# Performance work log

Measured on AMD Instinct MI355X. Metric: run time of the kernel, lower is better.

## Reference

```python
import jax, jax.numpy as jnp
import numpy as np

NQ = 10000   # num_q
N = 512      # n (seq len)
D = 512      # d (model dim)
H = 8        # attention heads
LW = 64      # local window
B = 16       # batch


def _mha(q, k, v, wi, bi, wo, bo, nh, mask=None):
    # torch nn.MultiheadAttention math (eval mode, dropout off), batch-first inputs
    Bq, S, d = q.shape
    hd = d // nh
    wq, wk, wv = jnp.split(wi, 3, axis=0)
    bq, bk, bv = jnp.split(bi, 3)

    def proj(x, w, b):
        y = x @ w.T + b
        return y.reshape(x.shape[0], x.shape[1], nh, hd).transpose(0, 2, 1, 3)  # [B,h,S,hd]

    Q = proj(q, wq, bq)
    K = proj(k, wk, bk)
    V = proj(v, wv, bv)
    s = jnp.einsum('bhqe,bhke->bhqk', Q, K) / jnp.sqrt(jnp.asarray(hd, q.dtype))
    if mask is not None:
        s = jnp.where(mask[None, None], -jnp.inf, s)
    w = jax.nn.softmax(s, axis=-1)
    o = jnp.einsum('bhqk,bhke->bhqe', w, V).transpose(0, 2, 1, 3).reshape(Bq, S, d)
    return o @ wo.T + bo, w.mean(axis=1)  # avg over heads like torch default


def _ln(x, g, b):
    m = x.mean(-1, keepdims=True)
    v = ((x - m) ** 2).mean(-1, keepdims=True)
    return (x - m) / jnp.sqrt(v + 1e-5) * g + b


def setup_inputs() -> dict:
    key = jax.random.key(0)
    ks = iter(jax.random.split(key, 40))
    f = lambda *sh: jax.random.normal(next(ks), sh, jnp.float32) * 0.02
    inp = {
        'q': jax.random.randint(next(ks), (B, N), 0, NQ, jnp.int32),
        'r': jax.random.randint(next(ks), (B, N), 0, 2, jnp.int32),
        'qry': jax.random.randint(next(ks), (B, N), 0, NQ, jnp.int32),
        'M_emb': f(2 * NQ, D),
        'E_emb': f(NQ, D),
        'P': f(N, D),
    }
    for nm in ['base', 'local', 'glob', 'cross']:
        inp[nm + '_in_w'] = f(3 * D, D)
        inp[nm + '_in_b'] = jnp.zeros((3 * D,), jnp.float32)
        inp[nm + '_out_w'] = f(D, D)
        inp[nm + '_out_b'] = jnp.zeros((D,), jnp.float32)
    inp['ln1_g'] = jnp.ones((D,), jnp.float32)
    inp['ln1_b'] = jnp.zeros((D,), jnp.float32)
    inp['w1'] = f(D, D)
    inp['b1'] = jnp.zeros((D,), jnp.float32)
    inp['w2'] = f(D, D)
    inp['b2'] = jnp.zeros((D,), jnp.float32)
    inp['ln2_g'] = jnp.ones((D,), jnp.float32)
    inp['ln2_b'] = jnp.zeros((D,), jnp.float32)
    inp['pred_w'] = f(1, D)
    inp['pred_b'] = jnp.zeros((1,), jnp.float32)
    return inp


def reference(q, r, qry, M_emb, E_emb, P,
              base_in_w, base_in_b, base_out_w, base_out_b,
              local_in_w, local_in_b, local_out_w, local_out_b,
              glob_in_w, glob_in_b, glob_out_w, glob_out_b,
              cross_in_w, cross_in_b, cross_out_w, cross_out_b,
              ln1_g, ln1_b, w1, b1, w2, b2, ln2_g, ln2_b, pred_w, pred_b):
    x = q + NQ * r
    M = M_emb[x] + P[None]          # [B,N,D], positional added as in torch code
    E = E_emb[qry]                  # [B,N,D]
    cm = jnp.triu(jnp.ones((N, N), bool), 1)

    S_base, attn_w = _mha(E, M, M, base_in_w, base_in_b, base_out_w, base_out_b, H, cm)
    S_base = _ln(S_base + M + E, ln1_g, ln1_b)

    lm = jnp.triu(jnp.ones((LW, LW), bool), 1)
    s_loc_in = S_base[:, -LW:, :]
    S_loc, _ = _mha(s_loc_in, s_loc_in, s_loc_in, local_in_w, local_in_b, local_out_w, local_out_b, H, lm)
    S_local = jnp.concatenate([jnp.zeros((S_base.shape[0], N - LW, D), S_base.dtype), S_loc], axis=1)

    S_global, _ = _mha(S_base, S_base, S_base, glob_in_w, glob_in_b, glob_out_w, glob_out_b, H, cm)
    S_cross, _ = _mha(S_base, S_local, S_local, cross_in_w, cross_in_b, cross_out_w, cross_out_b, H, None)

    S = S_base + S_local + S_global + S_cross
    F = jax.nn.relu(S @ w1.T + b1) @ w2.T + b2
    F = _ln(F + S, ln2_g, ln2_b)
    p = jax.nn.sigmoid(F @ pred_w.T + pred_b)[..., 0]   # [B,N]
    return p, attn_w
```

## Files before the change

kernel.cpp:

```cpp
#include <hip/hip_runtime.h>
#include <hip/hip_bf16.h>

#define D_MODEL 512
#define NHEAD 8
#define NSEQ 512
#define BATCH 16
#define LWIN 64
#define S2C 0.18033688f
#define L2E 1.44269504f

typedef short s16x8 __attribute__((ext_vector_type(8)));
typedef float f32x4 __attribute__((ext_vector_type(4)));

__device__ inline unsigned short f2bf(float f) {
    unsigned int u = __float_as_uint(f);
    u = (u + 0x7fffu + ((u >> 16) & 1u)) >> 16;
    return (unsigned short)u;
}
__device__ inline int sw4(int r) { return (r + (r >> 2)) & 3; }

#define GLD16(g, l) __builtin_amdgcn_global_load_lds( \
    (const __attribute__((address_space(1))) void*)(g), \
    (__attribute__((address_space(3))) void*)(l), 16, 0, 0)

struct WP { const float* p[10]; };
__global__ __launch_bounds__(256) void wconv_kernel(WP wp, unsigned short* __restrict__ Wb)
{
    const long e = ((long)blockIdx.x * 256 + threadIdx.x) * 4;
    const float* src; long loc;
    if (e < 3145728) { int rg = (int)(e / 786432); src = wp.p[rg]; loc = e - (long)rg * 786432; }
    else { long j = e - 3145728; int rg = (int)(j >> 18); src = wp.p[4 + rg]; loc = j - ((long)rg << 18); }
    float4 v = *(const float4*)(src + loc);
    ushort4 o; o.x = f2bf(v.x); o.y = f2bf(v.y); o.z = f2bf(v.z); o.w = f2bf(v.w);
    *(ushort4*)(Wb + e) = o;
}

__global__ __launch_bounds__(128) void embed_kernel(
    const int* __restrict__ q, const int* __restrict__ r, const int* __restrict__ qry,
    const float* __restrict__ M_emb, const float* __restrict__ E_emb,
    const float* __restrict__ P, float* __restrict__ Mf, float* __restrict__ Ef,
    unsigned short* __restrict__ Mb, unsigned short* __restrict__ Eb)
{
    const int t = blockIdx.x;
    const int n = t & (NSEQ - 1);
    const int x = q[t] + 10000 * r[t];
    const int e = qry[t];
    const int i = threadIdx.x;
    float4 a = ((const float4*)(M_emb + (long)x * D_MODEL))[i];
    float4 p4 = ((const float4*)(P + (long)n * D_MODEL))[i];
    float4 ev = ((const float4*)(E_emb + (long)e * D_MODEL))[i];
    float4 mv = make_float4(a.x + p4.x, a.y + p4.y, a.z + p4.z, a.w + p4.w);
    ((float4*)(Mf + (long)t * D_MODEL))[i] = mv;
    ((float4*)(Ef + (long)t * D_MODEL))[i] = ev;
    ushort4 mb; mb.x = f2bf(mv.x); mb.y = f2bf(mv.y); mb.z = f2bf(mv.z); mb.w = f2bf(mv.w);
    ushort4 eb; eb.x = f2bf(ev.x); eb.y = f2bf(ev.y); eb.z = f2bf(ev.z); eb.w = f2bf(ev.w);
    *(ushort4*)(Mb + (long)t * D_MODEL + i * 4) = mb;
    *(ushort4*)(Eb + (long)t * D_MODEL + i * 4) = eb;
}

__global__ __launch_bounds__(256) void zfill_kernel(unsigned short* __restrict__ p)
{
    const long i = ((long)blockIdx.x * 256 + threadIdx.x) * 8;
    *(uint4*)(p + i) = make_uint4(0u, 0u, 0u, 0u);
}

__global__ __launch_bounds__(256) void gemm_bf16(
    const unsigned short* __restrict__ A, const unsigned short* __restrict__ A2, int nsplit,
    const unsigned short* __restrict__ W, const float* __restrict__ bias,
    unsigned short* __restrict__ Cb, int ldcb, int crem,
    float* __restrict__ Cf, int ldcf,
    const float* __restrict__ r1, const float* __restrict__ r2, const float* __restrict__ tl,
    int relu, int arem)
{
    __shared__ __align__(16) unsigned short Sh[6144];
    unsigned short* As = Sh;
    unsigned short* Ws = Sh + 4096;
    float* Shf = (float*)Sh;

    const int tid = threadIdx.x, lane = tid & 63, wid = tid >> 6;
    const int m0 = blockIdx.y * 128, n0 = blockIdx.x * 64;
    const int lm = lane & 15;
    const int lq = lane >> 4;
    const unsigned short* Asel = (n0 >= nsplit) ? A2 : A;

    const int rlane = lane >> 2, clane = lane & 3;
    const int lr0 = wid * 16 + rlane;
    const int lr1 = 64 + lr0;
    int rgA0 = m0 + lr0, rgA1 = m0 + lr1;
    if (arem) {
        rgA0 = ((rgA0 >> 6) << 9) + (NSEQ - LWIN) + (rgA0 & 63);
        rgA1 = ((rgA1 >> 6) << 9) + (NSEQ - LWIN) + (rgA1 & 63);
    }
    const unsigned short* pA0 = Asel + (long)rgA0 * 512 + ((clane ^ sw4(lr0)) << 3);
    const unsigned short* pA1 = Asel + (long)rgA1 * 512 + ((clane ^ sw4(lr1)) << 3);
    const unsigned short* pW0 = W + (long)(n0 + lr0) * 512 + ((clane ^ sw4(lr0)) << 3);
    unsigned short* lA0 = As + (wid * 16) * 32;
    unsigned short* lA1 = As + (64 + wid * 16) * 32;
    unsigned short* lW0 = Ws + (wid * 16) * 32;

    f32x4 acc[2][4];
    #pragma unroll
    for (int i = 0; i < 2; ++i)
        #pragma unroll
        for (int j = 0; j < 4; ++j) acc[i][j] = (f32x4){0.f, 0.f, 0.f, 0.f};

    for (int k0 = 0; k0 < 512; k0 += 32) {
        __syncthreads();
        GLD16(pA0 + k0, lA0);
        GLD16(pA1 + k0, lA1);
        GLD16(pW0 + k0, lW0);
        __syncthreads();

        s16x8 af[2], wf[4];
        #pragma unroll
        for (int i = 0; i < 2; ++i) {
            const int ra = wid * 32 + i * 16 + lm;
            af[i] = *(const s16x8*)&As[ra * 32 + ((lq ^ sw4(ra)) << 3)];
        }
        #pragma unroll
        for (int j = 0; j < 4; ++j) {
            const int rw = j * 16 + lm;
            wf[j] = *(const s16x8*)&Ws[rw * 32 + ((lq ^ sw4(rw)) << 3)];
        }
        #pragma unroll
        for (int i = 0; i < 2; ++i)
            #pragma unroll
            for (int j = 0; j < 4; ++j)
                acc[i][j] = __builtin_amdgcn_mfma_f32_16x16x32_bf16(af[i], wf[j], acc[i][j], 0, 0, 0);
    }

    const int fr = lane & 15;
    const int q4 = (lane >> 4) * 4;
    for (int qtr = 0; qtr < 4; ++qtr) {
        __syncthreads();
        if (wid == qtr) {
            #pragma unroll
            for (int j = 0; j < 4; ++j) {
                const int lcol = j * 16 + fr;
                const float bv = bias[n0 + lcol];
                #pragma unroll
                for (int i = 0; i < 2; ++i) {
                    #pragma unroll
                    for (int rg = 0; rg < 4; ++rg) {
                        float v = acc[i][j][rg] + bv;
                        if (relu) v = fmaxf(v, 0.f);
                        Shf[(i * 16 + q4 + rg) * 68 + lcol] = v;
                    }
                }
            }
        }
        __syncthreads();
        #pragma unroll
        for (int it = 0; it < 2; ++it) {
            const int flat = it * 256 + tid;
            const int rowq = flat >> 4, k4 = flat & 15;
            const int grow = m0 + qtr * 32 + rowq;
            const int gcol = n0 + k4 * 4;
            float4 f = *(const float4*)&Shf[rowq * 68 + k4 * 4];
            if (r1) {
                float4 a = *(const float4*)(r1 + (long)grow * 512 + gcol);
                float4 b = *(const float4*)(r2 + (long)grow * 512 + gcol);
                f.x += a.x + b.x; f.y += a.y + b.y; f.z += a.z + b.z; f.w += a.w + b.w;
                const int n = grow & 511;
                if (n >= NSEQ - LWIN) {
                    float4 c = *(const float4*)(tl + ((long)(grow >> 9) * 64 + (n - (NSEQ - LWIN))) * 512 + gcol);
                    f.x += c.x; f.y += c.y; f.z += c.z; f.w += c.w;
                }
            }
            if (Cf) *(float4*)(Cf + (long)grow * ldcf + gcol) = f;
            if (Cb) {
                const int crow = crem ? (((grow >> 6) << 9) + (NSEQ - LWIN) + (grow & 63)) : grow;
                ushort4 u; u.x = f2bf(f.x); u.y = f2bf(f.y); u.z = f2bf(f.z); u.w = f2bf(f.w);
                *(ushort4*)(Cb + (long)crow * ldcb + gcol) = u;
            }
        }
    }
}

__global__ __launch_bounds__(256) void flash_mfma(
    const unsigned short* __restrict__ Q, const unsigned short* __restrict__ K,
    const unsigned short* __restrict__ V, unsigned short* __restrict__ O,
    float* __restrict__ stats, int Nq, int Nkv, int ldq, int ldkv, int causal)
{
    __shared__ __align__(16) unsigned short Ks[64 * 72];
    __shared__ __align__(16) unsigned short Pl[64 * 72];
    __shared__ __align__(16) unsigned int   Vt[64 * 36];

    const int tid = threadIdx.x, lane = tid & 63, w = tid >> 6;
    const int lm = lane & 15, lq = lane >> 4;
    const int h = blockIdx.y, b = blockIdx.z;
    const int nqt = Nq >> 6;
    const int qa = blockIdx.x, qb = nqt - 1 - qa;
    const bool single = (qa == qb);

    s16x8 aqA0, aqA1, aqB0, aqB1;
    {
        const unsigned short* qp = Q + ((long)b * Nq + qb * 64 + w * 16 + lm) * ldq + h * 64 + lq * 8;
        aqB0 = *(const s16x8*)qp; aqB1 = *(const s16x8*)(qp + 32);
    }
    if (!single) {
        const unsigned short* qp = Q + ((long)b * Nq + qa * 64 + w * 16 + lm) * ldq + h * 64 + lq * 8;
        aqA0 = *(const s16x8*)qp; aqA1 = *(const s16x8*)(qp + 32);
    }

    float mA = -INFINITY, lA = 0.f, mB = -INFINITY, lB = 0.f;
    f32x4 oA[4], oB[4];
    #pragma unroll
    for (int t = 0; t < 4; ++t) { oA[t] = (f32x4){0.f,0.f,0.f,0.f}; oB[t] = (f32x4){0.f,0.f,0.f,0.f}; }

    const int nkt = causal ? (qb + 1) : (Nkv >> 6);
    const int skey = tid >> 3, sd = (tid & 7) * 8;

    s16x8 kr0, kr1; uint4 vr0, vr1;
    {
        const long kb = ((long)b * Nkv) * ldkv + h * 64;
        kr0 = *(const s16x8*)(K + kb + (long)skey * ldkv + sd);
        kr1 = *(const s16x8*)(K + kb + (long)(skey + 32) * ldkv + sd);
        const unsigned short* vp = V + ((long)b * Nkv + 2 * skey) * ldkv + h * 64 + sd;
        vr0 = *(const uint4*)vp; vr1 = *(const uint4*)(vp + ldkv);
    }

    auto process = [&](s16x8 a0, s16x8 a1, float& m, float& l, f32x4* oacc, bool diag) {
        f32x4 sc[4];
        #pragma unroll
        for (int t = 0; t < 4; ++t) sc[t] = (f32x4){0.f,0.f,0.f,0.f};
        #pragma unroll
        for (int t = 0; t < 4; ++t) {
            s16x8 k0 = *(const s16x8*)&Ks[(t * 16 + lm) * 72 + lq * 8];
            s16x8 k1 = *(const s16x8*)&Ks[(t * 16 + lm) * 72 + lq * 8 + 32];
            sc[t] = __builtin_amdgcn_mfma_f32_16x16x32_bf16(k0, a0, sc[t], 0, 0, 0);
            sc[t] = __builtin_amdgcn_mfma_f32_16x16x32_bf16(k1, a1, sc[t], 0, 0, 0);
        }
        if (diag) {
            #pragma unroll
            for (int t = 0; t < 4; ++t)
                #pragma unroll
                for (int r = 0; r < 4; ++r)
                    if (t * 16 + lq * 4 + r > w * 16 + lm) sc[t][r] = -INFINITY;
        }
        float mt = sc[0][0];
        #pragma unroll
        for (int t = 0; t < 4; ++t)
            #pragma unroll
            for (int r = 0; r < 4; ++r) mt = fmaxf(mt, sc[t][r]);
        mt = fmaxf(mt, __shfl_xor(mt, 16));
        mt = fmaxf(mt, __shfl_xor(mt, 32));
        const float mn = fmaxf(m, mt);
        const float al = exp2f((m - mn) * S2C);
        float rs = 0.f;
        #pragma unroll
        for (int t = 0; t < 4; ++t)
            #pragma unroll
            for (int r = 0; r < 4; ++r) {
                float p = exp2f((sc[t][r] - mn) * S2C);
                sc[t][r] = p; rs += p;
            }
        rs += __shfl_xor(rs, 16);
        rs += __shfl_xor(rs, 32);
        m = mn; l = l * al + rs;
        #pragma unroll
        for (int t = 0; t < 4; ++t) oacc[t] *= al;
        #pragma unroll
        for (int t = 0; t < 4; ++t) {
            ushort4 u;
            u.x = f2bf(sc[t][0]); u.y = f2bf(sc[t][1]);
            u.z = f2bf(sc[t][2]); u.w = f2bf(sc[t][3]);
            *(ushort4*)&Pl[(w * 16 + lm) * 72 + t * 16 + lq * 4] = u;
        }
        #pragma unroll
        for (int ks = 0; ks < 2; ++ks) {
            s16x8 bp = *(const s16x8*)&Pl[(w * 16 + lm) * 72 + ks * 32 + lq * 8];
            #pragma unroll
            for (int t = 0; t < 4; ++t) {
                const int row = t * 16 + lm;
                const int pg = ((lq >> 1) + 2 * ks) ^ ((row >> 3) & 3);
                s16x8 av = *(const s16x8*)((const unsigned short*)Vt + row * 72 + pg * 16 + (lq & 1) * 8);
                oacc[t] = __builtin_amdgcn_mfma_f32_16x16x32_bf16(av, bp, oacc[t], 0, 0, 0);
            }
        }
    };

    for (int kt = 0; kt < nkt; ++kt) {
        __syncthreads();
        *(s16x8*)&Ks[skey * 72 + sd] = kr0;
        *(s16x8*)&Ks[(skey + 32) * 72 + sd] = kr1;
        {
            unsigned pw[8];
            pw[0] = (vr0.x & 0xffffu) | (vr1.x << 16);
            pw[1] = (vr0.x >> 16)     | (vr1.x & 0xffff0000u);
            pw[2] = (vr0.y & 0xffffu) | (vr1.y << 16);
            pw[3] = (vr0.y >> 16)     | (vr1.y & 0xffff0000u);
            pw[4] = (vr0.z & 0xffffu) | (vr1.z << 16);
            pw[5] = (vr0.z >> 16)     | (vr1.z & 0xffff0000u);
            pw[6] = (vr0.w & 0xffffu) | (vr1.w << 16);
            pw[7] = (vr0.w >> 16)     | (vr1.w & 0xffff0000u);
            #pragma unroll
            for (int j = 0; j < 8; ++j) {
                const int row = sd + j;
                const int col = (((skey >> 3) ^ ((row >> 3) & 3)) << 3) | (skey & 7);
                Vt[row * 36 + col] = pw[j];
            }
        }
        __syncthreads();
        if (kt + 1 < nkt) {
            const long kb = ((long)b * Nkv + (kt + 1) * 64) * ldkv + h * 64;
            kr0 = *(const s16x8*)(K + kb + (long)skey * ldkv + sd);
            kr1 = *(const s16x8*)(K + kb + (long)(skey + 32) * ldkv + sd);
            const unsigned short* vp = V + ((long)b * Nkv + (kt + 1) * 64 + 2 * skey) * ldkv + h * 64 + sd;
            vr0 = *(const uint4*)vp; vr1 = *(const uint4*)(vp + ldkv);
        }
        process(aqB0, aqB1, mB, lB, oB, causal && (kt == qb));
        if (!single && (!causal || kt <= qa))
            process(aqA0, aqA1, mA, lA, oA, causal && (kt == qa));
    }

    {
        const float inv = 1.0f / lB;
        const long orow = ((long)b * Nq + qb * 64 + w * 16 + lm) * D_MODEL + h * 64;
        #pragma unroll
        for (int t = 0; t < 4; ++t) {
            ushort4 u;
            u.x = f2bf(oB[t][0] * inv); u.y = f2bf(oB[t][1] * inv);
            u.z = f2bf(oB[t][2] * inv); u.w = f2bf(oB[t][3] * inv);
            *(ushort4*)(O + orow + t * 16 + lq * 4) = u;
        }
    }
    if (!single) {
        const float inv = 1.0f / lA;
        const long orow = ((long)b * Nq + qa * 64 + w * 16 + lm) * D_MODEL + h * 64;
        #pragma unroll
        for (int t = 0; t < 4; ++t) {
            ushort4 u;
            u.x = f2bf(oA[t][0] * inv); u.y = f2bf(oA[t][1] * inv);
            u.z = f2bf(oA[t][2] * inv); u.w = f2bf(oA[t][3] * inv);
            *(ushort4*)(O + orow + t * 16 + lq * 4) = u;
        }
    }
    if (stats && lq == 0) {
        long idx = (((long)b * NHEAD + h) * Nq + qb * 64 + w * 16 + lm) * 2;
        stats[idx] = mB * 0.125f; stats[idx + 1] = lB;
        if (!single) {
            idx = (((long)b * NHEAD + h) * Nq + qa * 64 + w * 16 + lm) * 2;
            stats[idx] = mA * 0.125f; stats[idx + 1] = lA;
        }
    }
}

__global__ __launch_bounds__(256) void attn_w_kernel(
    const unsigned short* __restrict__ Q, const unsigned short* __restrict__ K,
    const float* __restrict__ stats, float* __restrict__ AW, int ldq, int ldk)
{
    const int kt = blockIdx.x, qt = blockIdx.y, b = blockIdx.z;
    const int tid = threadIdx.x;
    if (kt > qt) {
        const int tx = tid & 15, ty = tid >> 4;
        #pragma unroll
        for (int i = 0; i < 4; ++i)
            *(float4*)(AW + ((long)b * NSEQ + qt * 64 + ty * 4 + i) * NSEQ + kt * 64 + tx * 4)
                = make_float4(0.f, 0.f, 0.f, 0.f);
        return;
    }
    __shared__ __align__(16) unsigned short Ks[64 * 72];
    const int lane = tid & 63, w = tid >> 6;
    const int lm = lane & 15, lq = lane >> 4;
    const int skey = tid >> 3, sd = (tid & 7) * 8;
    const long qrow = (long)b * NSEQ + qt * 64 + w * 16 + lm;

    f32x4 aw[4];
    #pragma unroll
    for (int t = 0; t < 4; ++t) aw[t] = (f32x4){0.f,0.f,0.f,0.f};

    for (int h = 0; h < NHEAD; ++h) {
        __syncthreads();
        {
            const long kb = ((long)b * NSEQ + kt * 64) * ldk + h * 64;
            *(s16x8*)&Ks[skey * 72 + sd] = *(const s16x8*)(K + kb + (long)skey * ldk + sd);
            *(s16x8*)&Ks[(skey + 32) * 72 + sd] = *(const s16x8*)(K + kb + (long)(skey + 32) * ldk + sd);
        }
        __syncthreads();
        s16x8 a0, a1;
        {
            const unsigned short* qp = Q + qrow * ldq + h * 64 + lq * 8;
            a0 = *(const s16x8*)qp; a1 = *(const s16x8*)(qp + 32);
        }
        f32x4 sc[4];
        #pragma unroll
        for (int t = 0; t < 4; ++t) sc[t] = (f32x4){0.f,0.f,0.f,0.f};
        #pragma unroll
        for (int t = 0; t < 4; ++t) {
            s16x8 k0 = *(const s16x8*)&Ks[(t * 16 + lm) * 72 + lq * 8];
            s16x8 k1 = *(const s16x8*)&Ks[(t * 16 + lm) * 72 + lq * 8 + 32];
            sc[t] = __builtin_amdgcn_mfma_f32_16x16x32_bf16(k0, a0, sc[t], 0, 0, 0);
            sc[t] = __builtin_amdgcn_mfma_f32_16x16x32_bf16(k1, a1, sc[t], 0, 0, 0);
        }
        float2 ml = *(const float2*)(stats + (((long)b * NHEAD + h) * NSEQ + qt * 64 + w * 16 + lm) * 2);
        const float mb2 = ml.x * L2E;
        const float sca = 0.125f / ml.y;
        #pragma unroll
        for (int t = 0; t < 4; ++t)
            #pragma unroll
            for (int r = 0; r < 4; ++r) {
                const bool masked = (kt == qt) && (t * 16 + lq * 4 + r > w * 16 + lm);
                if (!masked) aw[t][r] += exp2f(sc[t][r] * S2C - mb2) * sca;
            }
    }
    #pragma unroll
    for (int t = 0; t < 4; ++t)
        *(float4*)(AW + qrow * NSEQ + kt * 64 + t * 16 + lq * 4) = float4{aw[t][0], aw[t][1], aw[t][2], aw[t][3]};
}

__global__ __launch_bounds__(256) void ln_kernel(
    const float* __restrict__ X, const float* __restrict__ R1,
    const float* __restrict__ R2, const float* __restrict__ g,
    const float* __restrict__ bb, float* __restrict__ outf,
    unsigned short* __restrict__ outb,
    const float* __restrict__ pw, const float* __restrict__ pb,
    float* __restrict__ outp)
{
    const long row = blockIdx.x;
    const int tid = threadIdx.x;
    __shared__ float red[256];
    const long base = row * D_MODEL;
    float v0 = X[base + tid], v1 = X[base + tid + 256];
    if (R1) { v0 += R1[base + tid]; v1 += R1[base + tid + 256]; }
    if (R2) { v0 += R2[base + tid]; v1 += R2[base + tid + 256]; }
    red[tid] = v0 + v1; __syncthreads();
    for (int s = 128; s > 0; s >>= 1) {
        if (tid < s) red[tid] += red[tid + s];
        __syncthreads();
    }
    const float mean = red[0] * (1.f / 512.f);
    __syncthreads();
    const float d0 = v0 - mean, d1 = v1 - mean;
    red[tid] = d0 * d0 + d1 * d1; __syncthreads();
    for (int s = 128; s > 0; s >>= 1) {
        if (tid < s) red[tid] += red[tid + s];
        __syncthreads();
    }
    const float rstd = rsqrtf(red[0] * (1.f / 512.f) + 1e-5f);
    const float y0 = d0 * rstd * g[tid] + bb[tid];
    const float y1 = d1 * rstd * g[tid + 256] + bb[tid + 256];
    if (pw) {
        float s = y0 * pw[tid] + y1 * pw[tid + 256];
        __syncthreads();
        red[tid] = s; __syncthreads();
        for (int st = 128; st > 0; st >>= 1) {
            if (tid < st) red[tid] += red[tid + st];
            __syncthreads();
        }
        if (tid == 0) outp[row] = 1.f / (1.f + __expf(-(red[0] + pb[0])));
        return;
    }
    if (outf) { outf[base + tid] = y0; outf[base + tid + 256] = y1; }
    if (outb) { outb[base + tid] = f2bf(y0); outb[base + tid + 256] = f2bf(y1); }
}

extern "C" void kernel_launch(void* const* d_in, const int* in_sizes, int n_in,
                              void* d_out, int out_size, void* d_ws, size_t ws_size,
                              hipStream_t stream)
{
    const int*   q          = (const int*)d_in[0];
    const int*   r          = (const int*)d_in[1];
    const int*   qry        = (const int*)d_in[2];
    const float* M_emb      = (const float*)d_in[3];
    const float* E_emb      = (const float*)d_in[4];
    const float* P          = (const float*)d_in[5];
    const float* base_in_w  = (const float*)d_in[6];
    const float* base_in_b  = (const float*)d_in[7];
    const float* base_out_w = (const float*)d_in[8];
    const float* base_out_b = (const float*)d_in[9];
    const float* local_in_w = (const float*)d_in[10];
    const float* local_in_b = (const float*)d_in[11];
    const float* local_out_w= (const float*)d_in[12];
    const float* local_out_b= (const float*)d_in[13];
    const float* glob_in_w  = (const float*)d_in[14];
    const float* glob_in_b  = (const float*)d_in[15];
    const float* glob_out_w = (const float*)d_in[16];
    const float* glob_out_b = (const float*)d_in[17];
    const float* cross_in_w = (const float*)d_in[18];
    const float* cross_in_b = (const float*)d_in[19];
    const float* cross_out_w= (const float*)d_in[20];
    const float* cross_out_b= (const float*)d_in[21];
    const float* ln1_g      = (const float*)d_in[22];
    const float* ln1_b      = (const float*)d_in[23];
    const float* w1         = (const float*)d_in[24];
    const float* b1         = (const float*)d_in[25];
    const float* w2         = (const float*)d_in[26];
    const float* b2         = (const float*)d_in[27];
    const float* ln2_g      = (const float*)d_in[28];
    const float* ln2_b      = (const float*)d_in[29];
    const float* pred_w     = (const float*)d_in[30];
    const float* pred_b     = (const float*)d_in[31];
    float* out = (float*)d_out;

    char* p = (char*)d_ws;
    unsigned short* Wb = (unsigned short*)p; p += 4718592L * 2;
    unsigned short* B[11];
    for (int i = 0; i < 11; ++i) { B[i] = (unsigned short*)p; p += 8388608L; }
    unsigned short* Obl  = (unsigned short*)p; p += 1048576L;
    float* R[4];
    for (int i = 0; i < 4; ++i) { R[i] = (float*)p; p += 16777216L; }
    float* Tloc  = (float*)p; p += 2097152L;
    float* stats = (float*)p; p += 524288L;

    unsigned short* Mb = B[0];
    unsigned short* Eb = B[1];      unsigned short* Oc_b = B[1];
    unsigned short* QKVb = B[2];
    unsigned short* Sb_b = B[2];
    unsigned short* Ob  = B[5];
    unsigned short* Sbase_b  = B[6];
    unsigned short* Slocal_b = B[7];
    unsigned short* QKV3 = B[8];
    unsigned short* H1_b = B[8];
    float* Mf = R[0];
    float* Ef = R[1];       float* Sbuf_f   = R[1];
    float* Tb_f = R[2];     float* Sglobal_f= R[2];
    float* Sbase_f = R[3];  float* Fpre_f   = R[3];

    const long oBin = 0, oLin = 786432, oGin = 1572864, oCin = 2359296;
    const long oBout = 3145728, oLout = 3407872, oGout = 3670016, oCout = 3932160;
    const long oW1 = 4194304, oW2 = 4456448;
    const int BIG = 1 << 30;
    const unsigned short* NUS = nullptr;
    const float* NF = nullptr;

    dim3 gN512(8, 64), gN1536(24, 64);
    dim3 gL1536(24, 8), gL512(8, 8);
    dim3 fa_full(4, NHEAD, BATCH), fa_loc(1, NHEAD, BATCH);

    WP wp; wp.p[0] = base_in_w; wp.p[1] = local_in_w; wp.p[2] = glob_in_w; wp.p[3] = cross_in_w;
    wp.p[4] = base_out_w; wp.p[5] = local_out_w; wp.p[6] = glob_out_w; wp.p[7] = cross_out_w;
    wp.p[8] = w1; wp.p[9] = w2;
    wconv_kernel<<<4608, 256, 0, stream>>>(wp, Wb);
    zfill_kernel<<<2048, 256, 0, stream>>>(Slocal_b);

    embed_kernel<<<8192, 128, 0, stream>>>(q, r, qry, M_emb, E_emb, P, Mf, Ef, Mb, Eb);

    gemm_bf16<<<gN1536, 256, 0, stream>>>(Eb, Mb, 512, Wb + oBin, base_in_b,
        QKVb, 1536, 0, nullptr, 0, NF, NF, NF, 0, 0);
    flash_mfma<<<fa_full, 256, 0, stream>>>(QKVb, QKVb + 512, QKVb + 1024, Ob, stats, 512, 512, 1536, 1536, 1);
    attn_w_kernel<<<dim3(8, 8, BATCH), 256, 0, stream>>>(QKVb, QKVb + 512, stats, out + 8192, 1536, 1536);
    gemm_bf16<<<gN512, 256, 0, stream>>>(Ob, NUS, BIG, Wb + oBout, base_out_b,
        nullptr, 0, 0, Tb_f, 512, NF, NF, NF, 0, 0);
    ln_kernel<<<8192, 256, 0, stream>>>(Tb_f, Mf, Ef, ln1_g, ln1_b, Sbase_f, Sbase_b, NF, NF, nullptr);

    gemm_bf16<<<gL1536, 256, 0, stream>>>(Sbase_b, NUS, BIG, Wb + oLin, local_in_b,
        QKV3, 1536, 0, nullptr, 0, NF, NF, NF, 0, 1);
    flash_mfma<<<fa_loc, 256, 0, stream>>>(QKV3, QKV3 + 512, QKV3 + 1024, Obl, nullptr, 64, 64, 1536, 1536, 1);
    gemm_bf16<<<gL512, 256, 0, stream>>>(Obl, NUS, BIG, Wb + oLout, local_out_b,
        Slocal_b, 512, 1, Tloc, 512, NF, NF, NF, 0, 0);

    gemm_bf16<<<gN1536, 256, 0, stream>>>(Sbase_b, NUS, BIG, Wb + oGin, glob_in_b,
        QKV3, 1536, 0, nullptr, 0, NF, NF, NF, 0, 0);
    flash_mfma<<<fa_full, 256, 0, stream>>>(QKV3, QKV3 + 512, QKV3 + 1024, Ob, nullptr, 512, 512, 1536, 1536, 1);
    gemm_bf16<<<gN512, 256, 0, stream>>>(Ob, NUS, BIG, Wb + oGout, glob_out_b,
        nullptr, 0, 0, Sglobal_f, 512, NF, NF, NF, 0, 0);

    gemm_bf16<<<gN1536, 256, 0, stream>>>(Sbase_b, Slocal_b, 512, Wb + oCin, cross_in_b,
        QKVb, 1536, 0, nullptr, 0, NF, NF, NF, 0, 0);
    flash_mfma<<<fa_full, 256, 0, stream>>>(QKVb, QKVb + 512, QKVb + 1024, Oc_b, nullptr, 512, 512, 1536, 1536, 0);
    gemm_bf16<<<gN512, 256, 0, stream>>>(Oc_b, NUS, BIG, Wb + oCout, cross_out_b,
        Sb_b, 512, 0, Sbuf_f, 512, Sbase_f, Sglobal_f, Tloc, 0, 0);

    gemm_bf16<<<gN512, 256, 0, stream>>>(Sb_b, NUS, BIG, Wb + oW1, b1,
        H1_b, 512, 0, nullptr, 0, NF, NF, NF, 1, 0);
    gemm_bf16<<<gN512, 256, 0, stream>>>(H1_b, NUS, BIG, Wb + oW2, b2,
        nullptr, 0, 0, Fpre_f, 512, NF, NF, NF, 0, 0);
    ln_kernel<<<8192, 256, 0, stream>>>(Fpre_f, Sbuf_f, nullptr, ln2_g, ln2_b,
        nullptr, nullptr, pred_w, pred_b, out);
}
```

Before: 508.2 us.

## Merge independent launches: fused front kernel, batched local/global GEMMs and attention, fold residuals

```diff
diff --git a/kernel.cpp b/kernel.cpp
--- a/kernel.cpp
+++ b/kernel.cpp
@@ -24,76 +24,82 @@
     (__attribute__((address_space(3))) void*)(l), 16, 0, 0)
 
 struct WP { const float* p[10]; };
-__global__ __launch_bounds__(256) void wconv_kernel(WP wp, unsigned short* __restrict__ Wb)
-{
-    const long e = ((long)blockIdx.x * 256 + threadIdx.x) * 4;
-    const float* src; long loc;
-    if (e < 3145728) { int rg = (int)(e / 786432); src = wp.p[rg]; loc = e - (long)rg * 786432; }
-    else { long j = e - 3145728; int rg = (int)(j >> 18); src = wp.p[4 + rg]; loc = j - ((long)rg << 18); }
-    float4 v = *(const float4*)(src + loc);
-    ushort4 o; o.x = f2bf(v.x); o.y = f2bf(v.y); o.z = f2bf(v.z); o.w = f2bf(v.w);
-    *(ushort4*)(Wb + e) = o;
-}
-
-__global__ __launch_bounds__(128) void embed_kernel(
+
+__global__ __launch_bounds__(256) void front_kernel(
+    WP wp, unsigned short* __restrict__ Wb, unsigned short* __restrict__ Z,
     const int* __restrict__ q, const int* __restrict__ r, const int* __restrict__ qry,
     const float* __restrict__ M_emb, const float* __restrict__ E_emb,
     const float* __restrict__ P, float* __restrict__ Mf, float* __restrict__ Ef,
     unsigned short* __restrict__ Mb, unsigned short* __restrict__ Eb)
 {
-    const int t = blockIdx.x;
-    const int n = t & (NSEQ - 1);
-    const int x = q[t] + 10000 * r[t];
-    const int e = qry[t];
-    const int i = threadIdx.x;
-    float4 a = ((const float4*)(M_emb + (long)x * D_MODEL))[i];
-    float4 p4 = ((const float4*)(P + (long)n * D_MODEL))[i];
-    float4 ev = ((const float4*)(E_emb + (long)e * D_MODEL))[i];
-    float4 mv = make_float4(a.x + p4.x, a.y + p4.y, a.z + p4.z, a.w + p4.w);
-    ((float4*)(Mf + (long)t * D_MODEL))[i] = mv;
-    ((float4*)(Ef + (long)t * D_MODEL))[i] = ev;
-    ushort4 mb; mb.x = f2bf(mv.x); mb.y = f2bf(mv.y); mb.z = f2bf(mv.z); mb.w = f2bf(mv.w);
-    ushort4 eb; eb.x = f2bf(ev.x); eb.y = f2bf(ev.y); eb.z = f2bf(ev.z); eb.w = f2bf(ev.w);
-    *(ushort4*)(Mb + (long)t * D_MODEL + i * 4) = mb;
-    *(ushort4*)(Eb + (long)t * D_MODEL + i * 4) = eb;
-}
-
-__global__ __launch_bounds__(256) void zfill_kernel(unsigned short* __restrict__ p)
-{
-    const long i = ((long)blockIdx.x * 256 + threadIdx.x) * 8;
-    *(uint4*)(p + i) = make_uint4(0u, 0u, 0u, 0u);
-}
-
-__global__ __launch_bounds__(256) void gemm_bf16(
-    const unsigned short* __restrict__ A, const unsigned short* __restrict__ A2, int nsplit,
-    const unsigned short* __restrict__ W, const float* __restrict__ bias,
-    unsigned short* __restrict__ Cb, int ldcb, int crem,
-    float* __restrict__ Cf, int ldcf,
-    const float* __restrict__ r1, const float* __restrict__ r2, const float* __restrict__ tl,
-    int relu, int arem)
+    const int blk = blockIdx.x, tid = threadIdx.x;
+    if (blk < 4608) {
+        const long e = ((long)blk * 256 + tid) * 4;
+        const float* src; long loc;
+        if (e < 3145728) { int rg = (int)(e / 786432); src = wp.p[rg]; loc = e - (long)rg * 786432; }
+        else { long j = e - 3145728; int rg = (int)(j >> 18); src = wp.p[4 + rg]; loc = j - ((long)rg << 18); }
+        float4 v = *(const float4*)(src + loc);
+        ushort4 o; o.x = f2bf(v.x); o.y = f2bf(v.y); o.z = f2bf(v.z); o.w = f2bf(v.w);
+        *(ushort4*)(Wb + e) = o;
+    } else if (blk < 6656) {
+        const long i = ((long)(blk - 4608) * 256 + tid) * 8;
+        *(uint4*)(Z + i) = make_uint4(0u, 0u, 0u, 0u);
+    } else {
+        const int t = (blk - 6656) * 2 + (tid >> 7);
+        const int i = tid & 127;
+        const int n = t & (NSEQ - 1);
+        const int x = q[t] + 10000 * r[t];
+        const int e = qry[t];
+        float4 a = ((const float4*)(M_emb + (long)x * D_MODEL))[i];
+        float4 p4 = ((const float4*)(P + (long)n * D_MODEL))[i];
+        float4 ev = ((const float4*)(E_emb + (long)e * D_MODEL))[i];
+        float4 mv = make_float4(a.x + p4.x, a.y + p4.y, a.z + p4.z, a.w + p4.w);
+        ((float4*)(Mf + (long)t * D_MODEL))[i] = mv;
+        ((float4*)(Ef + (long)t * D_MODEL))[i] = ev;
+        ushort4 mb; mb.x = f2bf(mv.x); mb.y = f2bf(mv.y); mb.z = f2bf(mv.z); mb.w = f2bf(mv.w);
+        ushort4 eb; eb.x = f2bf(ev.x); eb.y = f2bf(ev.y); eb.z = f2bf(ev.z); eb.w = f2bf(ev.w);
+        *(ushort4*)(Mb + (long)t * D_MODEL + i * 4) = mb;
+        *(ushort4*)(Eb + (long)t * D_MODEL + i * 4) = eb;
+    }
+}
+
+struct GArgs {
+    const unsigned short* A; const unsigned short* A2; int nsplit;
+    const unsigned short* W; const float* bias;
+    unsigned short* Cb; int ldcb; int crem;
+    float* Cf; int ldcf;
+    const float* r1; const float* r2; const float* tl;
+    int relu; int arem;
+};
+
+__global__ __launch_bounds__(256) void gemm_bf16(GArgs g0, GArgs g1, int msplit)
 {
     __shared__ __align__(16) unsigned short Sh[6144];
     unsigned short* As = Sh;
     unsigned short* Ws = Sh + 4096;
     float* Shf = (float*)Sh;
 
+    int m0 = blockIdx.y * 128;
+    const GArgs& G = (m0 < msplit) ? g0 : g1;
+    if (m0 >= msplit) m0 -= msplit;
+
     const int tid = threadIdx.x, lane = tid & 63, wid = tid >> 6;
-    const int m0 = blockIdx.y * 128, n0 = blockIdx.x * 64;
+    const int n0 = blockIdx.x * 64;
     const int lm = lane & 15;
     const int lq = lane >> 4;
-    const unsigned short* Asel = (n0 >= nsplit) ? A2 : A;
+    const unsigned short* Asel = (n0 >= G.nsplit) ? G.A2 : G.A;
 
     const int rlane = lane >> 2, clane = lane & 3;
     const int lr0 = wid * 16 + rlane;
     const int lr1 = 64 + lr0;
     int rgA0 = m0 + lr0, rgA1 = m0 + lr1;
-    if (arem) {
+    if (G.arem) {
         rgA0 = ((rgA0 >> 6) << 9) + (NSEQ - LWIN) + (rgA0 & 63);
         rgA1 = ((rgA1 >> 6) << 9) + (NSEQ - LWIN) + (rgA1 & 63);
     }
     const unsigned short* pA0 = Asel + (long)rgA0 * 512 + ((clane ^ sw4(lr0)) << 3);
     const unsigned short* pA1 = Asel + (long)rgA1 * 512 + ((clane ^ sw4(lr1)) << 3);
-    const unsigned short* pW0 = W + (long)(n0 + lr0) * 512 + ((clane ^ sw4(lr0)) << 3);
+    const unsigned short* pW0 = G.W + (long)(n0 + lr0) * 512 + ((clane ^ sw4(lr0)) << 3);
     unsigned short* lA0 = As + (wid * 16) * 32;
     unsigned short* lA1 = As + (64 + wid * 16) * 32;
     unsigned short* lW0 = Ws + (wid * 16) * 32;
@@ -137,13 +143,13 @@
             #pragma unroll
             for (int j = 0; j < 4; ++j) {
                 const int lcol = j * 16 + fr;
-                const float bv = bias[n0 + lcol];
+                const float bv = G.bias[n0 + lcol];
                 #pragma unroll
                 for (int i = 0; i < 2; ++i) {
                     #pragma unroll
                     for (int rg = 0; rg < 4; ++rg) {
                         float v = acc[i][j][rg] + bv;
-                        if (relu) v = fmaxf(v, 0.f);
+                        if (G.relu) v = fmaxf(v, 0.f);
                         Shf[(i * 16 + q4 + rg) * 68 + lcol] = v;
                     }
                 }
@@ -157,49 +163,60 @@
             const int grow = m0 + qtr * 32 + rowq;
             const int gcol = n0 + k4 * 4;
             float4 f = *(const float4*)&Shf[rowq * 68 + k4 * 4];
-            if (r1) {
-                float4 a = *(const float4*)(r1 + (long)grow * 512 + gcol);
-                float4 b = *(const float4*)(r2 + (long)grow * 512 + gcol);
-                f.x += a.x + b.x; f.y += a.y + b.y; f.z += a.z + b.z; f.w += a.w + b.w;
+            if (G.r1) {
+                float4 a = *(const float4*)(G.r1 + (long)grow * 512 + gcol);
+                f.x += a.x; f.y += a.y; f.z += a.z; f.w += a.w;
+            }
+            if (G.r2) {
+                float4 b = *(const float4*)(G.r2 + (long)grow * 512 + gcol);
+                f.x += b.x; f.y += b.y; f.z += b.z; f.w += b.w;
+            }
+            if (G.tl) {
                 const int n = grow & 511;
                 if (n >= NSEQ - LWIN) {
-                    float4 c = *(const float4*)(tl + ((long)(grow >> 9) * 64 + (n - (NSEQ - LWIN))) * 512 + gcol);
+                    float4 c = *(const float4*)(G.tl + ((long)(grow >> 9) * 64 + (n - (NSEQ - LWIN))) * 512 + gcol);
                     f.x += c.x; f.y += c.y; f.z += c.z; f.w += c.w;
                 }
             }
-            if (Cf) *(float4*)(Cf + (long)grow * ldcf + gcol) = f;
-            if (Cb) {
-                const int crow = crem ? (((grow >> 6) << 9) + (NSEQ - LWIN) + (grow & 63)) : grow;
+            if (G.Cf) *(float4*)(G.Cf + (long)grow * G.ldcf + gcol) = f;
+            if (G.Cb) {
+                const int crow = G.crem ? (((grow >> 6) << 9) + (NSEQ - LWIN) + (grow & 63)) : grow;
                 ushort4 u; u.x = f2bf(f.x); u.y = f2bf(f.y); u.z = f2bf(f.z); u.w = f2bf(f.w);
-                *(ushort4*)(Cb + (long)crow * ldcb + gcol) = u;
-            }
-        }
-    }
-}
-
-__global__ __launch_bounds__(256) void flash_mfma(
-    const unsigned short* __restrict__ Q, const unsigned short* __restrict__ K,
-    const unsigned short* __restrict__ V, unsigned short* __restrict__ O,
-    float* __restrict__ stats, int Nq, int Nkv, int ldq, int ldkv, int causal)
+                *(ushort4*)(G.Cb + (long)crow * G.ldcb + gcol) = u;
+            }
+        }
+    }
+}
+
+struct FArgs {
+    const unsigned short* Q; const unsigned short* K; const unsigned short* V;
+    unsigned short* O; float* stats; int Nq, Nkv, ldq, ldkv, causal;
+};
+
+__global__ __launch_bounds__(256) void flash_mfma(FArgs f0, FArgs f1, int xsplit)
 {
     __shared__ __align__(16) unsigned short Ks[64 * 72];
     __shared__ __align__(16) unsigned short Pl[64 * 72];
     __shared__ __align__(16) unsigned int   Vt[64 * 36];
 
+    const FArgs& F = ((int)blockIdx.x < xsplit) ? f0 : f1;
+    const int bx = ((int)blockIdx.x < xsplit) ? blockIdx.x : (blockIdx.x - xsplit);
+
     const int tid = threadIdx.x, lane = tid & 63, w = tid >> 6;
     const int lm = lane & 15, lq = lane >> 4;
     const int h = blockIdx.y, b = blockIdx.z;
+    const int Nq = F.Nq, Nkv = F.Nkv, ldq = F.ldq, ldkv = F.ldkv, causal = F.causal;
     const int nqt = Nq >> 6;
-    const int qa = blockIdx.x, qb = nqt - 1 - qa;
+    const int qa = bx, qb = nqt - 1 - qa;
     const bool single = (qa == qb);
 
     s16x8 aqA0, aqA1, aqB0, aqB1;
     {
-        const unsigned short* qp = Q + ((long)b * Nq + qb * 64 + w * 16 + lm) * ldq + h * 64 + lq * 8;
+        const unsigned short* qp = F.Q + ((long)b * Nq + qb * 64 + w * 16 + lm) * ldq + h * 64 + lq * 8;
         aqB0 = *(const s16x8*)qp; aqB1 = *(const s16x8*)(qp + 32);
     }
     if (!single) {
-        const unsigned short* qp = Q + ((long)b * Nq + qa * 64 + w * 16 + lm) * ldq + h * 64 + lq * 8;
+        const unsigned short* qp = F.Q + ((long)b * Nq + qa * 64 + w * 16 + lm) * ldq + h * 64 + lq * 8;
         aqA0 = *(const s16x8*)qp; aqA1 = *(const s16x8*)(qp + 32);
     }
 
@@ -214,9 +231,9 @@
     s16x8 kr0, kr1; uint4 vr0, vr1;
     {
         const long kb = ((long)b * Nkv) * ldkv + h * 64;
-        kr0 = *(const s16x8*)(K + kb + (long)skey * ldkv + sd);
-        kr1 = *(const s16x8*)(K + kb + (long)(skey + 32) * ldkv + sd);
-        const unsigned short* vp = V + ((long)b * Nkv + 2 * skey) * ldkv + h * 64 + sd;
+        kr0 = *(const s16x8*)(F.K + kb + (long)skey * ldkv + sd);
+        kr1 = *(const s16x8*)(F.K + kb + (long)(skey + 32) * ldkv + sd);
+        const unsigned short* vp = F.V + ((long)b * Nkv + 2 * skey) * ldkv + h * 64 + sd;
         vr0 = *(const uint4*)vp; vr1 = *(const uint4*)(vp + ldkv);
     }
 
@@ -304,9 +321,9 @@
         __syncthreads();
         if (kt + 1 < nkt) {
             const long kb = ((long)b * Nkv + (kt + 1) * 64) * ldkv + h * 64;
-            kr0 = *(const s16x8*)(K + kb + (long)skey * ldkv + sd);
-            kr1 = *(const s16x8*)(K + kb + (long)(skey + 32) * ldkv + sd);
-            const unsigned short* vp = V + ((long)b * Nkv + (kt + 1) * 64 + 2 * skey) * ldkv + h * 64 + sd;
+            kr0 = *(const s16x8*)(F.K + kb + (long)skey * ldkv + sd);
+            kr1 = *(const s16x8*)(F.K + kb + (long)(skey + 32) * ldkv + sd);
+            const unsigned short* vp = F.V + ((long)b * Nkv + (kt + 1) * 64 + 2 * skey) * ldkv + h * 64 + sd;
             vr0 = *(const uint4*)vp; vr1 = *(const uint4*)(vp + ldkv);
         }
         process(aqB0, aqB1, mB, lB, oB, causal && (kt == qb));
@@ -322,7 +339,7 @@
             ushort4 u;
             u.x = f2bf(oB[t][0] * inv); u.y = f2bf(oB[t][1] * inv);
             u.z = f2bf(oB[t][2] * inv); u.w = f2bf(oB[t][3] * inv);
-            *(ushort4*)(O + orow + t * 16 + lq * 4) = u;
+            *(ushort4*)(F.O + orow + t * 16 + lq * 4) = u;
         }
     }
     if (!single) {
@@ -333,15 +350,15 @@
             ushort4 u;
             u.x = f2bf(oA[t][0] * inv); u.y = f2bf(oA[t][1] * inv);
             u.z = f2bf(oA[t][2] * inv); u.w = f2bf(oA[t][3] * inv);
-            *(ushort4*)(O + orow + t * 16 + lq * 4) = u;
-        }
-    }
-    if (stats && lq == 0) {
+            *(ushort4*)(F.O + orow + t * 16 + lq * 4) = u;
+        }
+    }
+    if (F.stats && lq == 0) {
         long idx = (((long)b * NHEAD + h) * Nq + qb * 64 + w * 16 + lm) * 2;
-        stats[idx] = mB * 0.125f; stats[idx + 1] = lB;
+        F.stats[idx] = mB * 0.125f; F.stats[idx + 1] = lB;
         if (!single) {
             idx = (((long)b * NHEAD + h) * Nq + qa * 64 + w * 16 + lm) * 2;
-            stats[idx] = mA * 0.125f; stats[idx + 1] = lA;
+            F.stats[idx] = mA * 0.125f; F.stats[idx + 1] = lA;
         }
     }
 }
@@ -497,7 +514,8 @@
     unsigned short* Wb = (unsigned short*)p; p += 4718592L * 2;
     unsigned short* B[11];
     for (int i = 0; i < 11; ++i) { B[i] = (unsigned short*)p; p += 8388608L; }
-    unsigned short* Obl  = (unsigned short*)p; p += 1048576L;
+    unsigned short* Obl   = (unsigned short*)p; p += 1048576L;
+    unsigned short* QKV3L = (unsigned short*)p; p += 3145728L;
     float* R[4];
     for (int i = 0; i < 4; ++i) { R[i] = (float*)p; p += 16777216L; }
     float* Tloc  = (float*)p; p += 2097152L;
@@ -524,48 +542,58 @@
     const unsigned short* NUS = nullptr;
     const float* NF = nullptr;
 
-    dim3 gN512(8, 64), gN1536(24, 64);
-    dim3 gL1536(24, 8), gL512(8, 8);
-    dim3 fa_full(4, NHEAD, BATCH), fa_loc(1, NHEAD, BATCH);
+    auto GA = [](const unsigned short* A, const unsigned short* A2, int nsplit,
+                 const unsigned short* W, const float* bias,
+                 unsigned short* Cb, int ldcb, int crem, float* Cf, int ldcf,
+                 const float* r1, const float* r2, const float* tl, int relu, int arem) {
+        GArgs g; g.A = A; g.A2 = A2; g.nsplit = nsplit; g.W = W; g.bias = bias;
+        g.Cb = Cb; g.ldcb = ldcb; g.crem = crem; g.Cf = Cf; g.ldcf = ldcf;
+        g.r1 = r1; g.r2 = r2; g.tl = tl; g.relu = relu; g.arem = arem; return g;
+    };
+    auto FA = [](const unsigned short* Q, const unsigned short* K, const unsigned short* V,
+                 unsigned short* O, float* stats, int Nq, int Nkv, int ldq, int ldkv, int causal) {
+        FArgs f; f.Q = Q; f.K = K; f.V = V; f.O = O; f.stats = stats;
+        f.Nq = Nq; f.Nkv = Nkv; f.ldq = ldq; f.ldkv = ldkv; f.causal = causal; return f;
+    };
 
     WP wp; wp.p[0] = base_in_w; wp.p[1] = local_in_w; wp.p[2] = glob_in_w; wp.p[3] = cross_in_w;
     wp.p[4] = base_out_w; wp.p[5] = local_out_w; wp.p[6] = glob_out_w; wp.p[7] = cross_out_w;
     wp.p[8] = w1; wp.p[9] = w2;
-    wconv_kernel<<<4608, 256, 0, stream>>>(wp, Wb);
-    zfill_kernel<<<2048, 256, 0, stream>>>(Slocal_b);
-
-    embed_kernel<<<8192, 128, 0, stream>>>(q, r, qry, M_emb, E_emb, P, Mf, Ef, Mb, Eb);
-
-    gemm_bf16<<<gN1536, 256, 0, stream>>>(Eb, Mb, 512, Wb + oBin, base_in_b,
-        QKVb, 1536, 0, nullptr, 0, NF, NF, NF, 0, 0);
-    flash_mfma<<<fa_full, 256, 0, stream>>>(QKVb, QKVb + 512, QKVb + 1024, Ob, stats, 512, 512, 1536, 1536, 1);
+    front_kernel<<<10752, 256, 0, stream>>>(wp, Wb, Slocal_b, q, r, qry, M_emb, E_emb, P, Mf, Ef, Mb, Eb);
+
+    GArgs gBase = GA(Eb, Mb, 512, Wb + oBin, base_in_b, QKVb, 1536, 0, nullptr, 0, NF, NF, NF, 0, 0);
+    gemm_bf16<<<dim3(24, 64), 256, 0, stream>>>(gBase, gBase, BIG);
+    FArgs fBase = FA(QKVb, QKVb + 512, QKVb + 1024, Ob, stats, 512, 512, 1536, 1536, 1);
+    flash_mfma<<<dim3(4, NHEAD, BATCH), 256, 0, stream>>>(fBase, fBase, BIG);
     attn_w_kernel<<<dim3(8, 8, BATCH), 256, 0, stream>>>(QKVb, QKVb + 512, stats, out + 8192, 1536, 1536);
-    gemm_bf16<<<gN512, 256, 0, stream>>>(Ob, NUS, BIG, Wb + oBout, base_out_b,
-        nullptr, 0, 0, Tb_f, 512, NF, NF, NF, 0, 0);
-    ln_kernel<<<8192, 256, 0, stream>>>(Tb_f, Mf, Ef, ln1_g, ln1_b, Sbase_f, Sbase_b, NF, NF, nullptr);
-
-    gemm_bf16<<<gL1536, 256, 0, stream>>>(Sbase_b, NUS, BIG, Wb + oLin, local_in_b,
-        QKV3, 1536, 0, nullptr, 0, NF, NF, NF, 0, 1);
-    flash_mfma<<<fa_loc, 256, 0, stream>>>(QKV3, QKV3 + 512, QKV3 + 1024, Obl, nullptr, 64, 64, 1536, 1536, 1);
-    gemm_bf16<<<gL512, 256, 0, stream>>>(Obl, NUS, BIG, Wb + oLout, local_out_b,
-        Slocal_b, 512, 1, Tloc, 512, NF, NF, NF, 0, 0);
-
-    gemm_bf16<<<gN1536, 256, 0, stream>>>(Sbase_b, NUS, BIG, Wb + oGin, glob_in_b,
-        QKV3, 1536, 0, nullptr, 0, NF, NF, NF, 0, 0);
-    flash_mfma<<<fa_full, 256, 0, stream>>>(QKV3, QKV3 + 512, QKV3 + 1024, Ob, nullptr, 512, 512, 1536, 1536, 1);
-    gemm_bf16<<<gN512, 256, 0, stream>>>(Ob, NUS, BIG, Wb + oGout, glob_out_b,
-        nullptr, 0, 0, Sglobal_f, 512, NF, NF, NF, 0, 0);
-
-    gemm_bf16<<<gN1536, 256, 0, stream>>>(Sbase_b, Slocal_b, 512, Wb + oCin, cross_in_b,
-        QKVb, 1536, 0, nullptr, 0, NF, NF, NF, 0, 0);
-    flash_mfma<<<fa_full, 256, 0, stream>>>(QKVb, QKVb + 512, QKVb + 1024, Oc_b, nullptr, 512, 512, 1536, 1536, 0);
-    gemm_bf16<<<gN512, 256, 0, stream>>>(Oc_b, NUS, BIG, Wb + oCout, cross_out_b,
-        Sb_b, 512, 0, Sbuf_f, 512, Sbase_f, Sglobal_f, Tloc, 0, 0);
-
-    gemm_bf16<<<gN512, 256, 0, stream>>>(Sb_b, NUS, BIG, Wb + oW1, b1,
-        H1_b, 512, 0, nullptr, 0, NF, NF, NF, 1, 0);
-    gemm_bf16<<<gN512, 256, 0, stream>>>(H1_b, NUS, BIG, Wb + oW2, b2,
-        nullptr, 0, 0, Fpre_f, 512, NF, NF, NF, 0, 0);
-    ln_kernel<<<8192, 256, 0, stream>>>(Fpre_f, Sbuf_f, nullptr, ln2_g, ln2_b,
+    GArgs gBo = GA(Ob, NUS, BIG, Wb + oBout, base_out_b, nullptr, 0, 0, Tb_f, 512, Mf, Ef, NF, 0, 0);
+    gemm_bf16<<<dim3(8, 64), 256, 0, stream>>>(gBo, gBo, BIG);
+    ln_kernel<<<8192, 256, 0, stream>>>(Tb_f, NF, NF, ln1_g, ln1_b, Sbase_f, Sbase_b, NF, NF, nullptr);
+
+    GArgs gGin = GA(Sbase_b, NUS, BIG, Wb + oGin, glob_in_b, QKV3, 1536, 0, nullptr, 0, NF, NF, NF, 0, 0);
+    GArgs gLin = GA(Sbase_b, NUS, BIG, Wb + oLin, local_in_b, QKV3L, 1536, 0, nullptr, 0, NF, NF, NF, 0, 1);
+    gemm_bf16<<<dim3(24, 72), 256, 0, stream>>>(gGin, gLin, 8192);
+
+    FArgs fGlob = FA(QKV3, QKV3 + 512, QKV3 + 1024, Ob, nullptr, 512, 512, 1536, 1536, 1);
+    FArgs fLoc  = FA(QKV3L, QKV3L + 512, QKV3L + 1024, Obl, nullptr, 64, 64, 1536, 1536, 1);
+    flash_mfma<<<dim3(5, NHEAD, BATCH), 256, 0, stream>>>(fGlob, fLoc, 4);
+
+    GArgs gGo = GA(Ob, NUS, BIG, Wb + oGout, glob_out_b, nullptr, 0, 0, Sglobal_f, 512, NF, NF, NF, 0, 0);
+    GArgs gLo = GA(Obl, NUS, BIG, Wb + oLout, local_out_b, Slocal_b, 512, 1, Tloc, 512, NF, NF, NF, 0, 0);
+    gemm_bf16<<<dim3(8, 72), 256, 0, stream>>>(gGo, gLo, 8192);
+
+    GArgs gCin = GA(Sbase_b, Slocal_b, 512, Wb + oCin, cross_in_b, QKVb, 1536, 0, nullptr, 0, NF, NF, NF, 0, 0);
+    gemm_bf16<<<dim3(24, 64), 256, 0, stream>>>(gCin, gCin, BIG);
+    FArgs fCross = FA(QKVb, QKVb + 512, QKVb + 1024, Oc_b, nullptr, 512, 512, 1536, 1536, 0);
+    flash_mfma<<<dim3(4, NHEAD, BATCH), 256, 0, stream>>>(fCross, fCross, BIG);
+    GArgs gCo = GA(Oc_b, NUS, BIG, Wb + oCout, cross_out_b, Sb_b, 512, 0, Sbuf_f, 512,
+                   Sbase_f, Sglobal_f, Tloc, 0, 0);
+    gemm_bf16<<<dim3(8, 64), 256, 0, stream>>>(gCo, gCo, BIG);
+
+    GArgs gF1 = GA(Sb_b, NUS, BIG, Wb + oW1, b1, H1_b, 512, 0, nullptr, 0, NF, NF, NF, 1, 0);
+    gemm_bf16<<<dim3(8, 64), 256, 0, stream>>>(gF1, gF1, BIG);
+    GArgs gF2 = GA(H1_b, NUS, BIG, Wb + oW2, b2, nullptr, 0, 0, Fpre_f, 512, Sbuf_f, NF, NF, 0, 0);
+    gemm_bf16<<<dim3(8, 64), 256, 0, stream>>>(gF2, gF2, BIG);
+    ln_kernel<<<8192, 256, 0, stream>>>(Fpre_f, NF, NF, ln2_g, ln2_b,
         nullptr, nullptr, pred_w, pred_b, out);
 }
```

New measurement: 497.0 us. -2.2%, faster.
